# Kernel tuning notes

Hardware: AMD Instinct MI355X
Metric: run time of the kernel (lower is better)

## Reference

```python
import jax, jax.numpy as jnp
import numpy as np

H_GRID, W_GRID = 32, 32
KH, KW = 7, 11
NUM_HEADS = 8


def local_window_mask(H, W, kh, kw):
    # Token (h,w) may attend to (h',w') iff |h-h'|<=kh//2 and |w-w'|<=kw//2
    # (equivalent to the padded/cropped construction in the torch module).
    hh = jnp.arange(H)
    ww = jnp.arange(W)
    ok_h = jnp.abs(hh[:, None] - hh[None, :]) <= kh // 2  # [H,H]
    ok_w = jnp.abs(ww[:, None] - ww[None, :]) <= kw // 2  # [W,W]
    ok = ok_h[:, None, :, None] & ok_w[None, :, None, :]  # [H,W,H,W]
    ok = ok.reshape(H * W, H * W)
    return jnp.where(ok, 0.0, -jnp.inf)[None, None]  # [1,1,N,N]


def setup_inputs() -> dict:
    key = jax.random.key(0)
    k1, k2, k3, k4, k5 = jax.random.split(key, 5)
    B, N, E = 8, H_GRID * W_GRID, 256
    return {
        "x": jax.random.normal(k1, (B, N, E), dtype=jnp.float32),
        "qkv_w": jax.random.normal(k2, (3 * E, E), dtype=jnp.float32) * 0.02,
        "qkv_b": jax.random.normal(k3, (3 * E,), dtype=jnp.float32) * 0.02,
        "proj_w": jax.random.normal(k4, (E, E), dtype=jnp.float32) * 0.02,
        "proj_b": jax.random.normal(k5, (E,), dtype=jnp.float32) * 0.02,
    }


def reference(x, qkv_w, qkv_b, proj_w, proj_b):
    B, N, E = x.shape
    dh = E // NUM_HEADS
    scale = E ** (-0.5)  # note: embed_dim scaling, as in the original module
    qkv = x @ qkv_w.T + qkv_b                       # [B,N,3E]
    qkv = qkv.reshape(B, N, 3, NUM_HEADS, dh).transpose(2, 0, 3, 1, 4)
    q, k, v = qkv[0] * scale, qkv[1], qkv[2]        # [B,H,N,dh]
    attn = jnp.einsum('bhnd,bhmd->bhnm', q, k)      # [B,H,N,N]
    attn = attn + local_window_mask(H_GRID, W_GRID, KH, KW)
    attn = jax.nn.softmax(attn, axis=-1)
    out = jnp.einsum('bhnm,bhmd->bhnd', attn, v)    # [B,H,N,dh]
    out = out.transpose(0, 2, 1, 3).reshape(B, N, E)
    return out @ proj_w.T + proj_b
```

## Files before the change

kernel.cpp:

```cpp
#include <hip/hip_runtime.h>
#include <math.h>

constexpr int Bb = 8;
constexpr int Ns = 1024;
constexpr int Es = 256;
constexpr int NH = 8;
constexpr int DH = 32;
constexpr int Mrows = Bb * Ns;
constexpr int NX = Mrows * Es;
constexpr int NP = Es * Es;

typedef __bf16 bf16x8 __attribute__((ext_vector_type(8)));
typedef float  f32x4  __attribute__((ext_vector_type(4)));
union U4B8 { uint4 u; bf16x8 b; unsigned short s[8]; };

__device__ __forceinline__ unsigned short f2bf(float f) {
    union { float f; unsigned u; } c; c.f = f;
    unsigned r = (c.u + 0x7FFFu + ((c.u >> 16) & 1u)) >> 16;
    return (unsigned short)r;
}
__device__ __forceinline__ float bf2f(unsigned short h) {
    union { unsigned u; float f; } c; c.u = ((unsigned)h) << 16;
    return c.f;
}

#define GLD 72
#define SST 228
#define PST 232
#define AOT 264

__global__ __launch_bounds__(256, 4)
void qkv_gemm(const float* __restrict__ x, const float* __restrict__ qkv_w,
              const float* __restrict__ qkv_b, const float* __restrict__ proj_w,
              unsigned short* __restrict__ qo, unsigned short* __restrict__ ko,
              unsigned short* __restrict__ vto, unsigned short* __restrict__ pwb)
{
    __shared__ unsigned short As[64 * GLD];
    __shared__ unsigned short Ws[64 * GLD];

    const int t = threadIdx.x;

    if (blockIdx.x >= 1536) {
        int i = ((int)(blockIdx.x - 1536) * 256 + t) * 4;
        float4 f = *(const float4*)(proj_w + i);
        ushort4 u;
        u.x = f2bf(f.x); u.y = f2bf(f.y); u.z = f2bf(f.z); u.w = f2bf(f.w);
        *(ushort4*)(pwb + i) = u;
        return;
    }

    const int m0 = (blockIdx.x & 127) * 64;
    const int j0 = (blockIdx.x >> 7) * 64;

    const int srow = t >> 2;
    const int scol = (t & 3) * 16;

    const int lane = t & 63;
    const int wave = t >> 6;
    const int wm = (wave & 1) * 32;
    const int wn = (wave >> 1) * 32;
    const int fm = lane & 15;
    const int fq = lane >> 4;

    f32x4 acc[2][2];
    #pragma unroll
    for (int i = 0; i < 2; i++)
        #pragma unroll
        for (int j = 0; j < 2; j++)
            acc[i][j] = (f32x4){0.f, 0.f, 0.f, 0.f};

    const float* Arow = x + (size_t)(m0 + srow) * Es;
    const float* Wrow = qkv_w + (size_t)(j0 + srow) * Es;

    for (int k0 = 0; k0 < Es; k0 += 64) {
        float4 av[4], wv[4];
        #pragma unroll
        for (int i = 0; i < 4; i++) {
            av[i] = *(const float4*)(Arow + k0 + scol + 4 * i);
            wv[i] = *(const float4*)(Wrow + k0 + scol + 4 * i);
        }
        U4B8 pa0, pa1, pw0, pw1;
        #pragma unroll
        for (int i = 0; i < 2; i++) {
            pa0.s[4*i+0] = f2bf(av[i].x);   pa0.s[4*i+1] = f2bf(av[i].y);
            pa0.s[4*i+2] = f2bf(av[i].z);   pa0.s[4*i+3] = f2bf(av[i].w);
            pa1.s[4*i+0] = f2bf(av[i+2].x); pa1.s[4*i+1] = f2bf(av[i+2].y);
            pa1.s[4*i+2] = f2bf(av[i+2].z); pa1.s[4*i+3] = f2bf(av[i+2].w);
            pw0.s[4*i+0] = f2bf(wv[i].x);   pw0.s[4*i+1] = f2bf(wv[i].y);
            pw0.s[4*i+2] = f2bf(wv[i].z);   pw0.s[4*i+3] = f2bf(wv[i].w);
            pw1.s[4*i+0] = f2bf(wv[i+2].x); pw1.s[4*i+1] = f2bf(wv[i+2].y);
            pw1.s[4*i+2] = f2bf(wv[i+2].z); pw1.s[4*i+3] = f2bf(wv[i+2].w);
        }
        __syncthreads();
        *(uint4*)&As[srow * GLD + scol]     = pa0.u;
        *(uint4*)&As[srow * GLD + scol + 8] = pa1.u;
        *(uint4*)&Ws[srow * GLD + scol]     = pw0.u;
        *(uint4*)&Ws[srow * GLD + scol + 8] = pw1.u;
        __syncthreads();
        #pragma unroll
        for (int ks = 0; ks < 64; ks += 32) {
            U4B8 af0, af1, bf0, bf1;
            af0.u = *(const uint4*)&As[(wm +      fm) * GLD + ks + fq * 8];
            af1.u = *(const uint4*)&As[(wm + 16 + fm) * GLD + ks + fq * 8];
            bf0.u = *(const uint4*)&Ws[(wn +      fm) * GLD + ks + fq * 8];
            bf1.u = *(const uint4*)&Ws[(wn + 16 + fm) * GLD + ks + fq * 8];
            acc[0][0] = __builtin_amdgcn_mfma_f32_16x16x32_bf16(af0.b, bf0.b, acc[0][0], 0, 0, 0);
            acc[0][1] = __builtin_amdgcn_mfma_f32_16x16x32_bf16(af0.b, bf1.b, acc[0][1], 0, 0, 0);
            acc[1][0] = __builtin_amdgcn_mfma_f32_16x16x32_bf16(af1.b, bf0.b, acc[1][0], 0, 0, 0);
            acc[1][1] = __builtin_amdgcn_mfma_f32_16x16x32_bf16(af1.b, bf1.b, acc[1][1], 0, 0, 0);
        }
    }

    #pragma unroll
    for (int mt = 0; mt < 2; mt++) {
        #pragma unroll
        for (int nt = 0; nt < 2; nt++) {
            #pragma unroll
            for (int r = 0; r < 4; r++) {
                int row = m0 + wm + mt * 16 + fq * 4 + r;
                int col = j0 + wn + nt * 16 + fm;
                float val = acc[mt][nt][r] + qkv_b[col];
                int part = col >> 8;
                int head = (col >> 5) & 7;
                int d = col & 31;
                int b = row >> 10;
                int n = row & 1023;
                int bh = b * NH + head;
                if (part == 0)
                    qo[((size_t)bh * Ns + n) * DH + d] = f2bf(val * 0.0625f);
                else if (part == 1)
                    ko[((size_t)bh * Ns + n) * DH + d] = f2bf(val);
                else
                    vto[((size_t)bh * DH + d) * Ns + n] = f2bf(val);
            }
        }
    }
}

__global__ __launch_bounds__(512, 2)
void attn_proj(const unsigned short* __restrict__ qb, const unsigned short* __restrict__ kb,
               const unsigned short* __restrict__ vtb, const unsigned short* __restrict__ pwb,
               const float* __restrict__ proj_b, float* __restrict__ out)
{
    __shared__ float S2[2][32 * SST];
    __shared__ unsigned short Pb2[2][32 * PST];
    __shared__ float Linv2[2][32];
    __shared__ unsigned short aot[32 * AOT];

    const int t  = threadIdx.x;
    const int g  = t >> 8;
    const int tl = t & 255;
    const int hq = blockIdx.x & 31;
    const int b  = blockIdx.x >> 5;

    float* S  = S2[g];
    unsigned short* Pb = Pb2[g];
    float* Linv = Linv2[g];

    const int lane = tl & 63;
    const int w    = tl >> 6;
    const int fm = lane & 15;
    const int fq = lane >> 4;
    const int qbase = (w & 1) * 16;
    const int sel   = w >> 1;
    const int dbase = (w >> 1) * 16;

    int n0c = (hq - 3) * 32;
    n0c = n0c < 0 ? 0 : (n0c > Ns - 224 ? Ns - 224 : n0c);

    for (int hi = 0; hi < 4; hi++) {
        const int h  = g + 2 * hi;
        const int bh = b * NH + h;

        const unsigned short* vrow = vtb + ((size_t)bh * DH + dbase + fm) * Ns;
        uint4 vpre[7];
        #pragma unroll
        for (int i = 0; i < 7; i++)
            vpre[i] = *(const uint4*)(vrow + n0c + i * 32 + fq * 8);

        U4B8 qa;
        qa.u = *(const uint4*)(qb + ((size_t)bh * Ns + hq * 32 + qbase + fm) * DH + fq * 8);

        #pragma unroll
        for (int i = 0; i < 7; i++) {
            int kt = sel + 2 * i;
            U4B8 kf;
            kf.u = *(const uint4*)(kb + ((size_t)bh * Ns + n0c + kt * 16 + fm) * DH + fq * 8);
            f32x4 s = __builtin_amdgcn_mfma_f32_16x16x32_bf16(qa.b, kf.b, (f32x4){0.f,0.f,0.f,0.f}, 0, 0, 0);
            #pragma unroll
            for (int r = 0; r < 4; r++)
                S[(qbase + fq * 4 + r) * SST + kt * 16 + fm] = s[r];
        }
        __syncthreads();

        const int sq = tl >> 3;
        const int l8 = tl & 7;
        float sv[28];
        float smax = -INFINITY;
        #pragma unroll
        for (int i = 0; i < 28; i++) {
            int j = l8 + 8 * i;
            int gg = n0c + j;
            int gh = gg >> 5, gw = gg & 31;
            int dh_ = gh - hq, dw_ = gw - sq;
            bool ok = (dh_ >= -3) && (dh_ <= 3) && (dw_ >= -5) && (dw_ <= 5);
            float xv = ok ? S[sq * SST + j] : -INFINITY;
            sv[i] = xv;
            smax = fmaxf(smax, xv);
        }
        #pragma unroll
        for (int m = 1; m < 8; m <<= 1) smax = fmaxf(smax, __shfl_xor(smax, m));

        float lsum = 0.f;
        #pragma unroll
        for (int i = 0; i < 28; i++) {
            float p = __expf(sv[i] - smax);
            unsigned short pu = f2bf(p);
            Pb[sq * PST + l8 + 8 * i] = pu;
            lsum += bf2f(pu);
        }
        #pragma unroll
        for (int m = 1; m < 8; m <<= 1) lsum += __shfl_xor(lsum, m);
        if (l8 == 0) Linv[sq] = 1.f / lsum;
        __syncthreads();

        f32x4 acc = (f32x4){0.f, 0.f, 0.f, 0.f};
        #pragma unroll
        for (int i = 0; i < 7; i++) {
            U4B8 pa, vb;
            pa.u = *(const uint4*)&Pb[(qbase + fm) * PST + i * 32 + fq * 8];
            vb.u = vpre[i];
            acc = __builtin_amdgcn_mfma_f32_16x16x32_bf16(pa.b, vb.b, acc, 0, 0, 0);
        }
        #pragma unroll
        for (int r = 0; r < 4; r++) {
            int qq = qbase + fq * 4 + r;
            aot[qq * AOT + h * DH + dbase + fm] = f2bf(acc[r] * Linv[qq]);
        }
        __syncthreads();
    }

    const int ww   = t >> 6;
    const int col0 = ww * 32;
    const int pl   = t & 63;
    const int pfm  = pl & 15;
    const int pfq  = pl >> 4;

    f32x4 pacc[2][2];
    #pragma unroll
    for (int i = 0; i < 2; i++)
        #pragma unroll
        for (int j = 0; j < 2; j++)
            pacc[i][j] = (f32x4){0.f, 0.f, 0.f, 0.f};

    #pragma unroll
    for (int k0 = 0; k0 < Es; k0 += 32) {
        U4B8 a0, a1, b0, b1;
        a0.u = *(const uint4*)&aot[(pfm)      * AOT + k0 + pfq * 8];
        a1.u = *(const uint4*)&aot[(16 + pfm) * AOT + k0 + pfq * 8];
        b0.u = *(const uint4*)(pwb + (size_t)(col0 + pfm)      * Es + k0 + pfq * 8);
        b1.u = *(const uint4*)(pwb + (size_t)(col0 + 16 + pfm) * Es + k0 + pfq * 8);
        pacc[0][0] = __builtin_amdgcn_mfma_f32_16x16x32_bf16(a0.b, b0.b, pacc[0][0], 0, 0, 0);
        pacc[0][1] = __builtin_amdgcn_mfma_f32_16x16x32_bf16(a0.b, b1.b, pacc[0][1], 0, 0, 0);
        pacc[1][0] = __builtin_amdgcn_mfma_f32_16x16x32_bf16(a1.b, b0.b, pacc[1][0], 0, 0, 0);
        pacc[1][1] = __builtin_amdgcn_mfma_f32_16x16x32_bf16(a1.b, b1.b, pacc[1][1], 0, 0, 0);
    }

    const int rowbase = b * Ns + hq * 32;
    #pragma unroll
    for (int mt = 0; mt < 2; mt++) {
        #pragma unroll
        for (int nt = 0; nt < 2; nt++) {
            #pragma unroll
            for (int r = 0; r < 4; r++) {
                int row = rowbase + mt * 16 + pfq * 4 + r;
                int col = col0 + nt * 16 + pfm;
                out[(size_t)row * Es + col] = pacc[mt][nt][r] + proj_b[col];
            }
        }
    }
}

extern "C" void kernel_launch(void* const* d_in, const int* in_sizes, int n_in,
                              void* d_out, int out_size, void* d_ws, size_t ws_size,
                              hipStream_t stream) {
    const float* x      = (const float*)d_in[0];
    const float* qkv_w  = (const float*)d_in[1];
    const float* qkv_b  = (const float*)d_in[2];
    const float* proj_w = (const float*)d_in[3];
    const float* proj_b = (const float*)d_in[4];
    float* out = (float*)d_out;

    unsigned short* qb  = (unsigned short*)d_ws;
    unsigned short* kb  = qb + NX;
    unsigned short* vtb = kb + NX;
    unsigned short* pwb = vtb + NX;

    qkv_gemm<<<dim3(1600), dim3(256), 0, stream>>>(
        x, qkv_w, qkv_b, proj_w, qb, kb, vtb, pwb);

    attn_proj<<<dim3(Bb * 32), dim3(512), 0, stream>>>(
        qb, kb, vtb, pwb, proj_b, out);
}
```

Before: 109.3 us.

## Split fused attention+projection into per-head attention and separate projection GEMM

Replaces the fused attn_proj kernel, which looped over four heads per block with 256 blocks, with a per-(batch, head, row) attention kernel of 2048 blocks that writes a bf16 attention output to workspace, followed by a separate tiled projection GEMM. Softmax is now computed directly from MFMA accumulator registers using cross-lane shuffles plus a small shared-memory max/sum exchange, so the fp32 score staging buffer is gone. The aim is more parallelism and occupancy than 256 blocks gave, and less shared-memory traffic. In exchange it adds a kernel launch and a global round-trip of the attention output.

New measurement: 104.9 us. 4.0% less time.

```diff
diff --git a/kernel.cpp b/kernel.cpp
--- a/kernel.cpp
+++ b/kernel.cpp
@@ -25,9 +25,7 @@
 }
 
 #define GLD 72
-#define SST 228
 #define PST 232
-#define AOT 264
 
 __global__ __launch_bounds__(256, 4)
 void qkv_gemm(const float* __restrict__ x, const float* __restrict__ qkv_w,
@@ -137,145 +135,191 @@
     }
 }
 
-__global__ __launch_bounds__(512, 2)
-void attn_proj(const unsigned short* __restrict__ qb, const unsigned short* __restrict__ kb,
-               const unsigned short* __restrict__ vtb, const unsigned short* __restrict__ pwb,
-               const float* __restrict__ proj_b, float* __restrict__ out)
+__global__ __launch_bounds__(256)
+void attn_mfma2(const unsigned short* __restrict__ qb, const unsigned short* __restrict__ kb,
+                const unsigned short* __restrict__ vtb, unsigned short* __restrict__ aob)
 {
-    __shared__ float S2[2][32 * SST];
-    __shared__ unsigned short Pb2[2][32 * PST];
-    __shared__ float Linv2[2][32];
-    __shared__ unsigned short aot[32 * AOT];
-
-    const int t  = threadIdx.x;
-    const int g  = t >> 8;
-    const int tl = t & 255;
-    const int hq = blockIdx.x & 31;
-    const int b  = blockIdx.x >> 5;
-
-    float* S  = S2[g];
-    unsigned short* Pb = Pb2[g];
-    float* Linv = Linv2[g];
-
-    const int lane = tl & 63;
-    const int w    = tl >> 6;
+    __shared__ unsigned short Pb[32 * PST];
+    __shared__ float pmax[2][32];
+    __shared__ float psum[2][32];
+
+    const int blk = blockIdx.x;
+    const int hq  = blk & 31;
+    const int bh  = blk >> 5;
+    const int t   = threadIdx.x;
+    const int lane = t & 63;
+    const int w    = t >> 6;
     const int fm = lane & 15;
     const int fq = lane >> 4;
+
+    int n0c = (hq - 3) * 32;
+    n0c = n0c < 0 ? 0 : (n0c > Ns - 224 ? Ns - 224 : n0c);
+
     const int qbase = (w & 1) * 16;
     const int sel   = w >> 1;
     const int dbase = (w >> 1) * 16;
 
-    int n0c = (hq - 3) * 32;
-    n0c = n0c < 0 ? 0 : (n0c > Ns - 224 ? Ns - 224 : n0c);
-
-    for (int hi = 0; hi < 4; hi++) {
-        const int h  = g + 2 * hi;
-        const int bh = b * NH + h;
-
-        const unsigned short* vrow = vtb + ((size_t)bh * DH + dbase + fm) * Ns;
-        uint4 vpre[7];
-        #pragma unroll
-        for (int i = 0; i < 7; i++)
-            vpre[i] = *(const uint4*)(vrow + n0c + i * 32 + fq * 8);
-
-        U4B8 qa;
-        qa.u = *(const uint4*)(qb + ((size_t)bh * Ns + hq * 32 + qbase + fm) * DH + fq * 8);
-
-        #pragma unroll
-        for (int i = 0; i < 7; i++) {
-            int kt = sel + 2 * i;
-            U4B8 kf;
-            kf.u = *(const uint4*)(kb + ((size_t)bh * Ns + n0c + kt * 16 + fm) * DH + fq * 8);
-            f32x4 s = __builtin_amdgcn_mfma_f32_16x16x32_bf16(qa.b, kf.b, (f32x4){0.f,0.f,0.f,0.f}, 0, 0, 0);
-            #pragma unroll
-            for (int r = 0; r < 4; r++)
-                S[(qbase + fq * 4 + r) * SST + kt * 16 + fm] = s[r];
-        }
+    const unsigned short* vrow = vtb + ((size_t)bh * DH + dbase + fm) * Ns;
+    uint4 vpre[7];
+    #pragma unroll
+    for (int i = 0; i < 7; i++)
+        vpre[i] = *(const uint4*)(vrow + n0c + i * 32 + fq * 8);
+
+    U4B8 qa;
+    qa.u = *(const uint4*)(qb + ((size_t)bh * Ns + hq * 32 + qbase + fm) * DH + fq * 8);
+
+    f32x4 sv[7];
+    #pragma unroll
+    for (int i = 0; i < 7; i++) {
+        int kt = sel + 2 * i;
+        U4B8 kf;
+        kf.u = *(const uint4*)(kb + ((size_t)bh * Ns + n0c + kt * 16 + fm) * DH + fq * 8);
+        sv[i] = __builtin_amdgcn_mfma_f32_16x16x32_bf16(qa.b, kf.b, (f32x4){0.f,0.f,0.f,0.f}, 0, 0, 0);
+    }
+
+    float mx[4] = {-INFINITY, -INFINITY, -INFINITY, -INFINITY};
+    #pragma unroll
+    for (int i = 0; i < 7; i++) {
+        int g = n0c + (sel + 2 * i) * 16 + fm;
+        int gh = g >> 5, gw = g & 31;
+        int dhh = gh - hq;
+        bool okh = (dhh >= -3) && (dhh <= 3);
+        #pragma unroll
+        for (int r = 0; r < 4; r++) {
+            int qc = qbase + fq * 4 + r;
+            int dww = gw - qc;
+            bool ok = okh && (dww >= -5) && (dww <= 5);
+            float s = ok ? sv[i][r] : -INFINITY;
+            sv[i][r] = s;
+            mx[r] = fmaxf(mx[r], s);
+        }
+    }
+    #pragma unroll
+    for (int r = 0; r < 4; r++)
+        #pragma unroll
+        for (int m = 1; m < 16; m <<= 1)
+            mx[r] = fmaxf(mx[r], __shfl_xor(mx[r], m));
+    if (fm == 0) {
+        #pragma unroll
+        for (int r = 0; r < 4; r++)
+            pmax[sel][qbase + fq * 4 + r] = mx[r];
+    }
+    __syncthreads();
+
+    float M[4];
+    #pragma unroll
+    for (int r = 0; r < 4; r++) {
+        int qc = qbase + fq * 4 + r;
+        M[r] = fmaxf(pmax[0][qc], pmax[1][qc]);
+    }
+
+    float sm[4] = {0.f, 0.f, 0.f, 0.f};
+    #pragma unroll
+    for (int i = 0; i < 7; i++) {
+        int kt = sel + 2 * i;
+        #pragma unroll
+        for (int r = 0; r < 4; r++) {
+            float p = __expf(sv[i][r] - M[r]);
+            unsigned short pu = f2bf(p);
+            Pb[(qbase + fq * 4 + r) * PST + kt * 16 + fm] = pu;
+            sm[r] += bf2f(pu);
+        }
+    }
+    #pragma unroll
+    for (int r = 0; r < 4; r++)
+        #pragma unroll
+        for (int m = 1; m < 16; m <<= 1)
+            sm[r] += __shfl_xor(sm[r], m);
+    if (fm == 0) {
+        #pragma unroll
+        for (int r = 0; r < 4; r++)
+            psum[sel][qbase + fq * 4 + r] = sm[r];
+    }
+    __syncthreads();
+
+    f32x4 acc = (f32x4){0.f, 0.f, 0.f, 0.f};
+    #pragma unroll
+    for (int i = 0; i < 7; i++) {
+        U4B8 pa, vb;
+        pa.u = *(const uint4*)&Pb[(qbase + fm) * PST + i * 32 + fq * 8];
+        vb.u = vpre[i];
+        acc = __builtin_amdgcn_mfma_f32_16x16x32_bf16(pa.b, vb.b, acc, 0, 0, 0);
+    }
+
+    const int b = bh >> 3, h = bh & 7;
+    #pragma unroll
+    for (int r = 0; r < 4; r++) {
+        int qq = qbase + fq * 4 + r;
+        float inv = 1.f / (psum[0][qq] + psum[1][qq]);
+        aob[((size_t)(b * Ns) + hq * 32 + qq) * Es + h * DH + dbase + fm] = f2bf(acc[r] * inv);
+    }
+}
+
+__global__ __launch_bounds__(256, 4)
+void proj_gemm(const unsigned short* __restrict__ A, const unsigned short* __restrict__ Wb,
+               const float* __restrict__ bias, float* __restrict__ out)
+{
+    __shared__ unsigned short As[64 * GLD];
+    __shared__ unsigned short Ws[64 * GLD];
+
+    const int t = threadIdx.x;
+    const int m0 = (blockIdx.x & 127) * 64;
+    const int j0 = (blockIdx.x >> 7) * 64;
+
+    const int srow = t >> 2;
+    const int scol = (t & 3) * 16;
+
+    const int lane = t & 63;
+    const int wave = t >> 6;
+    const int wm = (wave & 1) * 32;
+    const int wn = (wave >> 1) * 32;
+    const int fm = lane & 15;
+    const int fq = lane >> 4;
+
+    f32x4 acc[2][2];
+    #pragma unroll
+    for (int i = 0; i < 2; i++)
+        #pragma unroll
+        for (int j = 0; j < 2; j++)
+            acc[i][j] = (f32x4){0.f, 0.f, 0.f, 0.f};
+
+    const unsigned short* Arow = A + (size_t)(m0 + srow) * Es;
+    const unsigned short* Wrow = Wb + (size_t)(j0 + srow) * Es;
+
+    for (int k0 = 0; k0 < Es; k0 += 64) {
+        uint4 a0 = *(const uint4*)(Arow + k0 + scol);
+        uint4 a1 = *(const uint4*)(Arow + k0 + scol + 8);
+        uint4 w0 = *(const uint4*)(Wrow + k0 + scol);
+        uint4 w1 = *(const uint4*)(Wrow + k0 + scol + 8);
         __syncthreads();
-
-        const int sq = tl >> 3;
-        const int l8 = tl & 7;
-        float sv[28];
-        float smax = -INFINITY;
-        #pragma unroll
-        for (int i = 0; i < 28; i++) {
-            int j = l8 + 8 * i;
-            int gg = n0c + j;
-            int gh = gg >> 5, gw = gg & 31;
-            int dh_ = gh - hq, dw_ = gw - sq;
-            bool ok = (dh_ >= -3) && (dh_ <= 3) && (dw_ >= -5) && (dw_ <= 5);
-            float xv = ok ? S[sq * SST + j] : -INFINITY;
-            sv[i] = xv;
-            smax = fmaxf(smax, xv);
-        }
-        #pragma unroll
-        for (int m = 1; m < 8; m <<= 1) smax = fmaxf(smax, __shfl_xor(smax, m));
-
-        float lsum = 0.f;
-        #pragma unroll
-        for (int i = 0; i < 28; i++) {
-            float p = __expf(sv[i] - smax);
-            unsigned short pu = f2bf(p);
-            Pb[sq * PST + l8 + 8 * i] = pu;
-            lsum += bf2f(pu);
-        }
-        #pragma unroll
-        for (int m = 1; m < 8; m <<= 1) lsum += __shfl_xor(lsum, m);
-        if (l8 == 0) Linv[sq] = 1.f / lsum;
+        *(uint4*)&As[srow * GLD + scol]     = a0;
+        *(uint4*)&As[srow * GLD + scol + 8] = a1;
+        *(uint4*)&Ws[srow * GLD + scol]     = w0;
+        *(uint4*)&Ws[srow * GLD + scol + 8] = w1;
         __syncthreads();
-
-        f32x4 acc = (f32x4){0.f, 0.f, 0.f, 0.f};
-        #pragma unroll
-        for (int i = 0; i < 7; i++) {
-            U4B8 pa, vb;
-            pa.u = *(const uint4*)&Pb[(qbase + fm) * PST + i * 32 + fq * 8];
-            vb.u = vpre[i];
-            acc = __builtin_amdgcn_mfma_f32_16x16x32_bf16(pa.b, vb.b, acc, 0, 0, 0);
-        }
-        #pragma unroll
-        for (int r = 0; r < 4; r++) {
-            int qq = qbase + fq * 4 + r;
-            aot[qq * AOT + h * DH + dbase + fm] = f2bf(acc[r] * Linv[qq]);
-        }
-        __syncthreads();
-    }
-
-    const int ww   = t >> 6;
-    const int col0 = ww * 32;
-    const int pl   = t & 63;
-    const int pfm  = pl & 15;
-    const int pfq  = pl >> 4;
-
-    f32x4 pacc[2][2];
-    #pragma unroll
-    for (int i = 0; i < 2; i++)
-        #pragma unroll
-        for (int j = 0; j < 2; j++)
-            pacc[i][j] = (f32x4){0.f, 0.f, 0.f, 0.f};
-
-    #pragma unroll
-    for (int k0 = 0; k0 < Es; k0 += 32) {
-        U4B8 a0, a1, b0, b1;
-        a0.u = *(const uint4*)&aot[(pfm)      * AOT + k0 + pfq * 8];
-        a1.u = *(const uint4*)&aot[(16 + pfm) * AOT + k0 + pfq * 8];
-        b0.u = *(const uint4*)(pwb + (size_t)(col0 + pfm)      * Es + k0 + pfq * 8);
-        b1.u = *(const uint4*)(pwb + (size_t)(col0 + 16 + pfm) * Es + k0 + pfq * 8);
-        pacc[0][0] = __builtin_amdgcn_mfma_f32_16x16x32_bf16(a0.b, b0.b, pacc[0][0], 0, 0, 0);
-        pacc[0][1] = __builtin_amdgcn_mfma_f32_16x16x32_bf16(a0.b, b1.b, pacc[0][1], 0, 0, 0);
-        pacc[1][0] = __builtin_amdgcn_mfma_f32_16x16x32_bf16(a1.b, b0.b, pacc[1][0], 0, 0, 0);
-        pacc[1][1] = __builtin_amdgcn_mfma_f32_16x16x32_bf16(a1.b, b1.b, pacc[1][1], 0, 0, 0);
-    }
-
-    const int rowbase = b * Ns + hq * 32;
+        #pragma unroll
+        for (int ks = 0; ks < 64; ks += 32) {
+            U4B8 af0, af1, bf0, bf1;
+            af0.u = *(const uint4*)&As[(wm +      fm) * GLD + ks + fq * 8];
+            af1.u = *(const uint4*)&As[(wm + 16 + fm) * GLD + ks + fq * 8];
+            bf0.u = *(const uint4*)&Ws[(wn +      fm) * GLD + ks + fq * 8];
+            bf1.u = *(const uint4*)&Ws[(wn + 16 + fm) * GLD + ks + fq * 8];
+            acc[0][0] = __builtin_amdgcn_mfma_f32_16x16x32_bf16(af0.b, bf0.b, acc[0][0], 0, 0, 0);
+            acc[0][1] = __builtin_amdgcn_mfma_f32_16x16x32_bf16(af0.b, bf1.b, acc[0][1], 0, 0, 0);
+            acc[1][0] = __builtin_amdgcn_mfma_f32_16x16x32_bf16(af1.b, bf0.b, acc[1][0], 0, 0, 0);
+            acc[1][1] = __builtin_amdgcn_mfma_f32_16x16x32_bf16(af1.b, bf1.b, acc[1][1], 0, 0, 0);
+        }
+    }
+
     #pragma unroll
     for (int mt = 0; mt < 2; mt++) {
         #pragma unroll
         for (int nt = 0; nt < 2; nt++) {
             #pragma unroll
             for (int r = 0; r < 4; r++) {
-                int row = rowbase + mt * 16 + pfq * 4 + r;
-                int col = col0 + nt * 16 + pfm;
-                out[(size_t)row * Es + col] = pacc[mt][nt][r] + proj_b[col];
+                int row = m0 + wm + mt * 16 + fq * 4 + r;
+                int col = j0 + wn + nt * 16 + fm;
+                out[(size_t)row * Es + col] = acc[mt][nt][r] + bias[col];
             }
         }
     }
@@ -295,10 +339,13 @@
     unsigned short* kb  = qb + NX;
     unsigned short* vtb = kb + NX;
     unsigned short* pwb = vtb + NX;
+    unsigned short* aob = pwb + NP;
 
     qkv_gemm<<<dim3(1600), dim3(256), 0, stream>>>(
         x, qkv_w, qkv_b, proj_w, qb, kb, vtb, pwb);
 
-    attn_proj<<<dim3(Bb * 32), dim3(512), 0, stream>>>(
-        qb, kb, vtb, pwb, proj_b, out);
-}
+    attn_mfma2<<<dim3(Bb * NH * 32), dim3(256), 0, stream>>>(qb, kb, vtb, aob);
+
+    proj_gemm<<<dim3(Mrows / 64 * (Es / 64)), dim3(256), 0, stream>>>(
+        aob, pwb, proj_b, out);
+}
```
